# Performance work log

Hardware: AMD Instinct MI355X
Metric: run time of the kernel (lower is better)

The kernel has to match this reference:

```python
import jax, jax.numpy as jnp
import numpy as np

DT = 0.03125                                   # ray-march step size
NSTEPS = int(np.ceil(2.0 * np.sqrt(3.0) / DT)) # enough steps to cross the [-1,1]^3 cube diagonal (=111)


def trilinear_sample(vol, pos):
    """vol: [C, D, Hv, Wv]; pos: [H, W, 3] xyz in [-1,1] (grid_sample convention,
    align_corners=True). Returns [C, H, W]."""
    D, Hv, Wv = vol.shape[1], vol.shape[2], vol.shape[3]

    def axis(g, n):
        g = jnp.clip((g + 1.0) * 0.5 * (n - 1), 0.0, n - 1.0)
        i0 = jnp.minimum(jnp.floor(g).astype(jnp.int32), n - 2)
        return i0, i0 + 1, (g - i0)[None]  # frac broadcast over channel dim

    x0, x1, fx = axis(pos[..., 0], Wv)
    y0, y1, fy = axis(pos[..., 1], Hv)
    z0, z1, fz = axis(pos[..., 2], D)

    def g(z, y, x):
        return vol[:, z, y, x]  # [C, H, W]

    c00 = g(z0, y0, x0) * (1 - fx) + g(z0, y0, x1) * fx
    c01 = g(z0, y1, x0) * (1 - fx) + g(z0, y1, x1) * fx
    c10 = g(z1, y0, x0) * (1 - fx) + g(z1, y0, x1) * fx
    c11 = g(z1, y1, x0) * (1 - fx) + g(z1, y1, x1) * fx
    c0 = c00 * (1 - fy) + c01 * fy
    c1 = c10 * (1 - fy) + c11 * fy
    return c0 * (1 - fz) + c1 * fz


def setup_inputs() -> dict:
    key = jax.random.key(0)
    B, H, W, D = 2, 256, 256, 128
    camrot = jnp.tile(jnp.eye(3, dtype=jnp.float32)[None], (B, 1, 1))
    campos = jnp.tile(jnp.array([[0.0, 0.0, -2.5]], dtype=jnp.float32), (B, 1))
    focal = jnp.full((B, 2), 300.0, dtype=jnp.float32)
    princpt = jnp.full((B, 2), 128.0, dtype=jnp.float32)
    ys, xs = jnp.meshgrid(jnp.arange(H, dtype=jnp.float32),
                          jnp.arange(W, dtype=jnp.float32), indexing='ij')
    pixelcoords = jnp.tile(jnp.stack([xs, ys], axis=-1)[None], (B, 1, 1, 1))
    volume = jax.random.uniform(key, (B, 4, D, D, D), dtype=jnp.float32)
    return dict(camrot=camrot, campos=campos, focal=focal, princpt=princpt,
                pixelcoords=pixelcoords, volume=volume)


def reference(camrot, campos, focal, princpt, pixelcoords, volume):
    # camera rays: pixel -> camera -> world (camrot^T applied, as in torch sum over dim=-2)
    raydir = (pixelcoords - princpt[:, None, None, :]) / focal[:, None, None, :]
    raydir = jnp.concatenate([raydir, jnp.ones_like(raydir[..., :1])], axis=-1)
    raydir = jnp.einsum('bij,bhwi->bhwj', camrot, raydir)
    raydir = raydir / jnp.sqrt(jnp.sum(raydir ** 2, axis=-1, keepdims=True))

    # ray-AABB intersection with [-1,1]^3 (no grad, as in torch.no_grad())
    t1 = (-1.0 - campos[:, None, None, :]) / raydir
    t2 = (1.0 - campos[:, None, None, :]) / raydir
    tmin = jnp.maximum(jnp.minimum(t1[..., 0], t2[..., 0]),
                       jnp.maximum(jnp.minimum(t1[..., 1], t2[..., 1]),
                                   jnp.minimum(t1[..., 2], t2[..., 2])))
    tmax = jnp.minimum(jnp.maximum(t1[..., 0], t2[..., 0]),
                       jnp.minimum(jnp.maximum(t1[..., 1], t2[..., 1]),
                                   jnp.maximum(t1[..., 2], t2[..., 2])))
    hit = tmin < tmax
    t0 = jax.lax.stop_gradient(jnp.maximum(jnp.where(hit, tmin, 0.0), 0.0))

    raypos = campos[:, None, None, :] + raydir * t0[..., None]  # [B,H,W,3]
    B, H, W = raypos.shape[:3]
    rayrgb = jnp.zeros((B, 3, H, W), raypos.dtype)
    rayalpha = jnp.zeros((B, 1, H, W), raypos.dtype)

    def step(carry, _):
        raypos, rayrgb, rayalpha = carry
        valid = jnp.all((raypos > -1.0) & (raypos < 1.0), axis=-1).astype(raypos.dtype)
        samp = jax.vmap(trilinear_sample)(volume, raypos)  # [B,4,H,W]
        contrib = (jnp.minimum(rayalpha + samp[:, 3:4] * DT, 1.0) - rayalpha) * valid[:, None]
        rayrgb = rayrgb + samp[:, :3] * contrib
        rayalpha = rayalpha + contrib
        raypos = raypos + raydir * DT
        return (raypos, rayrgb, rayalpha), None

    (_, rayrgb, rayalpha), _ = jax.lax.scan(step, (raypos, rayrgb, rayalpha),
                                            None, length=NSTEPS)
    return jnp.concatenate([rayrgb, rayalpha], axis=1)  # [B,4,H,W]
```

## Files before the change

### kernel.cpp

```cpp
#include <hip/hip_runtime.h>
#include <math.h>

#pragma clang fp contract(off)

#define DT 0.03125f
#define NSTEPS 111

__device__ __forceinline__ float4 lerp4(float4 a, float4 b, float w) {
#pragma clang fp contract(off)
    float wa = 1.0f - w;
    float4 r;
    r.x = a.x * wa + b.x * w;
    r.y = a.y * wa + b.y * w;
    r.z = a.z * wa + b.z * w;
    r.w = a.w * wa + b.w * w;
    return r;
}


__global__ __launch_bounds__(256) void repack4_kernel(const float* __restrict__ vol,
                                                      float4* __restrict__ out,
                                                      long spatial) {
    long q = (long)blockIdx.x * blockDim.x + threadIdx.x;
    long nq = spatial >> 2;
    if (q >= nq) return;
    long b = blockIdx.y;
    const float* p = vol + b * 4 * spatial + (q << 2);
    float4 c0 = *(const float4*)(p);
    float4 c1 = *(const float4*)(p + spatial);
    float4 c2 = *(const float4*)(p + 2 * spatial);
    float4 c3 = *(const float4*)(p + 3 * spatial);
    float4* o = out + b * spatial + (q << 2);
    o[0] = make_float4(c0.x, c1.x, c2.x, c3.x);
    o[1] = make_float4(c0.y, c1.y, c2.y, c3.y);
    o[2] = make_float4(c0.z, c1.z, c2.z, c3.z);
    o[3] = make_float4(c0.w, c1.w, c2.w, c3.w);
}

__global__ __launch_bounds__(256) void repack_kernel(const float* __restrict__ vol,
                                                     float4* __restrict__ out,
                                                     long total, long spatial) {
    long idx = (long)blockIdx.x * blockDim.x + threadIdx.x;
    if (idx >= total) return;
    long b = idx / spatial;
    long s = idx - b * spatial;
    const float* p = vol + b * 4 * spatial + s;
    float4 v;
    v.x = p[0];
    v.y = p[spatial];
    v.z = p[2 * spatial];
    v.w = p[3 * spatial];
    out[idx] = v;
}


__device__ __forceinline__ int voxel_base(float posx, float posy, float posz,
                                          int D, float gmax, int zstride,
                                          float& fx, float& fy, float& fz) {
#pragma clang fp contract(off)
    float gx = fminf(fmaxf((posx + 1.0f) * 0.5f * gmax, 0.0f), gmax);
    float gy = fminf(fmaxf((posy + 1.0f) * 0.5f * gmax, 0.0f), gmax);
    float gz = fminf(fmaxf((posz + 1.0f) * 0.5f * gmax, 0.0f), gmax);
    int ix0 = (int)floorf(gx); if (ix0 > D - 2) ix0 = D - 2;
    int iy0 = (int)floorf(gy); if (iy0 > D - 2) iy0 = D - 2;
    int iz0 = (int)floorf(gz); if (iz0 > D - 2) iz0 = D - 2;
    fx = gx - (float)ix0;
    fy = gy - (float)iy0;
    fz = gz - (float)iz0;
    return iz0 * zstride + iy0 * D + ix0;
}

__device__ __forceinline__ void load8(const float4* __restrict__ v4, int base,
                                      int D, int zstride, float4* c) {
    c[0] = v4[base];
    c[1] = v4[base + 1];
    c[2] = v4[base + D];
    c[3] = v4[base + D + 1];
    c[4] = v4[base + zstride];
    c[5] = v4[base + zstride + 1];
    c[6] = v4[base + zstride + D];
    c[7] = v4[base + zstride + D + 1];
}

__device__ __forceinline__ void accum_step(const float4* c, float fx, float fy, float fz,
                                           float& accr, float& accg, float& accb,
                                           float& alpha) {
#pragma clang fp contract(off)
    float4 c00 = lerp4(c[0], c[1], fx);
    float4 c01 = lerp4(c[2], c[3], fx);
    float4 c10 = lerp4(c[4], c[5], fx);
    float4 c11 = lerp4(c[6], c[7], fx);
    float4 c0 = lerp4(c00, c01, fy);
    float4 c1 = lerp4(c10, c11, fy);
    float4 samp = lerp4(c0, c1, fz);
    float contrib = fminf(alpha + samp.w * DT, 1.0f) - alpha;
    accr = accr + samp.x * contrib;
    accg = accg + samp.y * contrib;
    accb = accb + samp.z * contrib;
    alpha = alpha + contrib;
}

__global__ __launch_bounds__(256, 1) void raymarch_pipe_kernel(
        const float* __restrict__ camrot, const float* __restrict__ campos,
        const float* __restrict__ focal, const float* __restrict__ princpt,
        const float* __restrict__ pixelcoords, const float4* __restrict__ vol4,
        float* __restrict__ out, int B, int H, int W, int D) {
#pragma clang fp contract(off)
    int x = blockIdx.x * blockDim.x + threadIdx.x;
    int y = blockIdx.y * blockDim.y + threadIdx.y;
    int b = blockIdx.z;
    if (x >= W || y >= H) return;

    long pidx = (((long)b * H + y) * W + x) * 2;
    float px = pixelcoords[pidx];
    float py = pixelcoords[pidx + 1];
    const float* R = camrot + b * 9;
    float cpx = campos[b * 3 + 0], cpy = campos[b * 3 + 1], cpz = campos[b * 3 + 2];
    float flx = focal[b * 2 + 0], fly = focal[b * 2 + 1];
    float prx = princpt[b * 2 + 0], pry = princpt[b * 2 + 1];

    float rx = (px - prx) / flx;
    float ry = (py - pry) / fly;
    float rz = 1.0f;
    float dx = R[0] * rx + R[3] * ry + R[6] * rz;
    float dy = R[1] * rx + R[4] * ry + R[7] * rz;
    float dz = R[2] * rx + R[5] * ry + R[8] * rz;
    float ss = dx * dx;
    ss = ss + dy * dy;
    ss = ss + dz * dz;
    float nrm = sqrtf(ss);
    dx = dx / nrm; dy = dy / nrm; dz = dz / nrm;

    float t1x = (-1.0f - cpx) / dx, t2x = (1.0f - cpx) / dx;
    float t1y = (-1.0f - cpy) / dy, t2y = (1.0f - cpy) / dy;
    float t1z = (-1.0f - cpz) / dz, t2z = (1.0f - cpz) / dz;
    float tmin = fmaxf(fminf(t1x, t2x), fmaxf(fminf(t1y, t2y), fminf(t1z, t2z)));
    float tmax = fminf(fmaxf(t1x, t2x), fminf(fmaxf(t1y, t2y), fmaxf(t1z, t2z)));
    bool hit = tmin < tmax;
    float t0 = fmaxf(hit ? tmin : 0.0f, 0.0f);

    float posx = cpx + dx * t0;
    float posy = cpy + dy * t0;
    float posz = cpz + dz * t0;
    float stx = dx * DT, sty = dy * DT, stz = dz * DT;

    int n = 0;
    float e0x = 0.0f, e0y = 0.0f, e0z = 0.0f;
    {
        float sx = posx, sy = posy, sz = posz;
        int firstv = -1;
        for (int s = 0; s < NSTEPS; ++s) {
            bool valid = (sx > -1.0f) && (sx < 1.0f) &&
                         (sy > -1.0f) && (sy < 1.0f) &&
                         (sz > -1.0f) && (sz < 1.0f);
            if (valid) {
                if (firstv < 0) { firstv = s; e0x = sx; e0y = sy; e0z = sz; }
                n++;
            } else if (firstv >= 0) {
                break;
            }
            sx = sx + stx; sy = sy + sty; sz = sz + stz;
        }
    }

    float accr = 0.0f, accg = 0.0f, accb = 0.0f, alpha = 0.0f;
    float gmax = (float)(D - 1);
    int zstride = D * D;
    int spatial = zstride * D;
    const float4* v4b = vol4 + (long)b * spatial;

    if (n > 0) {
        float pxx = e0x, pyy = e0y, pzz = e0z;
        float fxA, fyA, fzA, fxB = 0.f, fyB = 0.f, fzB = 0.f;
        float4 A[8], Bv[8];

        int baseA = voxel_base(pxx, pyy, pzz, D, gmax, zstride, fxA, fyA, fzA);
        load8(v4b, baseA, D, zstride, A);
        pxx = pxx + stx; pyy = pyy + sty; pzz = pzz + stz;

        if (n > 1) {
            int baseB = voxel_base(pxx, pyy, pzz, D, gmax, zstride, fxB, fyB, fzB);
            load8(v4b, baseB, D, zstride, Bv);
            pxx = pxx + stx; pyy = pyy + sty; pzz = pzz + stz;
        }

        int i = 0;
        for (; i + 2 < n; i += 2) {
            accum_step(A, fxA, fyA, fzA, accr, accg, accb, alpha);
            int baseA2 = voxel_base(pxx, pyy, pzz, D, gmax, zstride, fxA, fyA, fzA);
            load8(v4b, baseA2, D, zstride, A);
            pxx = pxx + stx; pyy = pyy + sty; pzz = pzz + stz;

            accum_step(Bv, fxB, fyB, fzB, accr, accg, accb, alpha);
            int baseB2 = voxel_base(pxx, pyy, pzz, D, gmax, zstride, fxB, fyB, fzB);
            load8(v4b, baseB2, D, zstride, Bv);
            pxx = pxx + stx; pyy = pyy + sty; pzz = pzz + stz;
        }
        if (i < n) { accum_step(A, fxA, fyA, fzA, accr, accg, accb, alpha); i++; }
        if (i < n) { accum_step(Bv, fxB, fyB, fzB, accr, accg, accb, alpha); }
    }

    long hw = (long)H * W;
    long o = (long)b * 4 * hw + (long)y * W + x;
    out[o] = accr;
    out[o + hw] = accg;
    out[o + 2 * hw] = accb;
    out[o + 3 * hw] = alpha;
}

__global__ __launch_bounds__(256) void raymarch_simple_kernel(
        const float* __restrict__ camrot, const float* __restrict__ campos,
        const float* __restrict__ focal, const float* __restrict__ princpt,
        const float* __restrict__ pixelcoords, const float* __restrict__ vol,
        float* __restrict__ out, int B, int H, int W, int D) {
#pragma clang fp contract(off)
    int x = blockIdx.x * blockDim.x + threadIdx.x;
    int y = blockIdx.y * blockDim.y + threadIdx.y;
    int b = blockIdx.z;
    if (x >= W || y >= H) return;

    long pidx = (((long)b * H + y) * W + x) * 2;
    float px = pixelcoords[pidx];
    float py = pixelcoords[pidx + 1];
    const float* R = camrot + b * 9;
    float cpx = campos[b * 3 + 0], cpy = campos[b * 3 + 1], cpz = campos[b * 3 + 2];
    float flx = focal[b * 2 + 0], fly = focal[b * 2 + 1];
    float prx = princpt[b * 2 + 0], pry = princpt[b * 2 + 1];

    float rx = (px - prx) / flx;
    float ry = (py - pry) / fly;
    float rz = 1.0f;
    float dx = R[0] * rx + R[3] * ry + R[6] * rz;
    float dy = R[1] * rx + R[4] * ry + R[7] * rz;
    float dz = R[2] * rx + R[5] * ry + R[8] * rz;
    float ss = dx * dx;
    ss = ss + dy * dy;
    ss = ss + dz * dz;
    float nrm = sqrtf(ss);
    dx = dx / nrm; dy = dy / nrm; dz = dz / nrm;

    float t1x = (-1.0f - cpx) / dx, t2x = (1.0f - cpx) / dx;
    float t1y = (-1.0f - cpy) / dy, t2y = (1.0f - cpy) / dy;
    float t1z = (-1.0f - cpz) / dz, t2z = (1.0f - cpz) / dz;
    float tmin = fmaxf(fminf(t1x, t2x), fmaxf(fminf(t1y, t2y), fminf(t1z, t2z)));
    float tmax = fminf(fmaxf(t1x, t2x), fminf(fmaxf(t1y, t2y), fmaxf(t1z, t2z)));
    bool hit = tmin < tmax;
    float t0 = fmaxf(hit ? tmin : 0.0f, 0.0f);

    float posx = cpx + dx * t0;
    float posy = cpy + dy * t0;
    float posz = cpz + dz * t0;
    float stx = dx * DT, sty = dy * DT, stz = dz * DT;

    float accr = 0.0f, accg = 0.0f, accb = 0.0f, alpha = 0.0f;
    float gmax = (float)(D - 1);
    long spatial = (long)D * D * D;
    long zstride = (long)D * D;
    const float* vb = vol + (long)b * 4 * spatial;

    bool entered = false;
    for (int s = 0; s < NSTEPS; ++s) {
        bool valid = (posx > -1.0f) && (posx < 1.0f) &&
                     (posy > -1.0f) && (posy < 1.0f) &&
                     (posz > -1.0f) && (posz < 1.0f);
        if (valid) {
            entered = true;
            float gx = fminf(fmaxf((posx + 1.0f) * 0.5f * gmax, 0.0f), gmax);
            float gy = fminf(fmaxf((posy + 1.0f) * 0.5f * gmax, 0.0f), gmax);
            float gz = fminf(fmaxf((posz + 1.0f) * 0.5f * gmax, 0.0f), gmax);
            int ix0 = (int)floorf(gx); if (ix0 > D - 2) ix0 = D - 2;
            int iy0 = (int)floorf(gy); if (iy0 > D - 2) iy0 = D - 2;
            int iz0 = (int)floorf(gz); if (iz0 > D - 2) iz0 = D - 2;
            float fx = gx - (float)ix0;
            float fy = gy - (float)iy0;
            float fz = gz - (float)iz0;

            long s000 = (long)iz0 * zstride + (long)iy0 * D + ix0;
            float4 c000, c001, c010, c011, c100, c101, c110, c111;
            #define FETCH(dst, off) { long o_ = (off); \
                dst.x = vb[o_]; dst.y = vb[o_ + spatial]; \
                dst.z = vb[o_ + 2 * spatial]; dst.w = vb[o_ + 3 * spatial]; }
            FETCH(c000, s000);
            FETCH(c001, s000 + 1);
            FETCH(c010, s000 + D);
            FETCH(c011, s000 + D + 1);
            FETCH(c100, s000 + zstride);
            FETCH(c101, s000 + zstride + 1);
            FETCH(c110, s000 + zstride + D);
            FETCH(c111, s000 + zstride + D + 1);
            #undef FETCH
            float4 c00 = lerp4(c000, c001, fx);
            float4 c01 = lerp4(c010, c011, fx);
            float4 c10 = lerp4(c100, c101, fx);
            float4 c11 = lerp4(c110, c111, fx);
            float4 c0 = lerp4(c00, c01, fy);
            float4 c1 = lerp4(c10, c11, fy);
            float4 samp = lerp4(c0, c1, fz);

            float contrib = fminf(alpha + samp.w * DT, 1.0f) - alpha;
            accr = accr + samp.x * contrib;
            accg = accg + samp.y * contrib;
            accb = accb + samp.z * contrib;
            alpha = alpha + contrib;
            if (alpha >= 1.0f) break;
        } else if (entered) {
            break;
        }
        posx = posx + stx; posy = posy + sty; posz = posz + stz;
    }

    long hw = (long)H * W;
    long o = (long)b * 4 * hw + (long)y * W + x;
    out[o] = accr;
    out[o + hw] = accg;
    out[o + 2 * hw] = accb;
    out[o + 3 * hw] = alpha;
}

extern "C" void kernel_launch(void* const* d_in, const int* in_sizes, int n_in,
                              void* d_out, int out_size, void* d_ws, size_t ws_size,
                              hipStream_t stream) {
    const float* camrot = (const float*)d_in[0];
    const float* campos = (const float*)d_in[1];
    const float* focal = (const float*)d_in[2];
    const float* princpt = (const float*)d_in[3];
    const float* pixelcoords = (const float*)d_in[4];
    const float* volume = (const float*)d_in[5];
    float* out = (float*)d_out;

    int B = in_sizes[0] / 9;
    long spatial = (long)in_sizes[5] / (B * 4);
    int D = (int)lround(cbrt((double)spatial));
    while ((long)D * D * D > spatial) D--;
    while ((long)(D + 1) * (D + 1) * (D + 1) <= spatial) D++;
    long hw = (long)in_sizes[4] / (B * 2);
    int H = (int)lround(sqrt((double)hw));
    int W = H;

    size_t need = (size_t)B * spatial * 4 * sizeof(float);
    dim3 blk(16, 16, 1);
    dim3 grd((W + 15) / 16, (H + 15) / 16, B);

    if (ws_size >= need) {
        if ((spatial & 3) == 0) {
            long nq = spatial >> 2;
            dim3 rgrd((unsigned)((nq + 255) / 256), B, 1);
            repack4_kernel<<<rgrd, dim3(256), 0, stream>>>(volume, (float4*)d_ws, spatial);
        } else {
            long total = (long)B * spatial;
            repack_kernel<<<dim3((unsigned)((total + 255) / 256)), dim3(256), 0, stream>>>(
                volume, (float4*)d_ws, total, spatial);
        }
        raymarch_pipe_kernel<<<grd, blk, 0, stream>>>(camrot, campos, focal, princpt,
                                                      pixelcoords, (const float4*)d_ws,
                                                      out, B, H, W, D);
    } else {
        raymarch_simple_kernel<<<grd, blk, 0, stream>>>(camrot, campos, focal, princpt,
                                                        pixelcoords, volume,
                                                        out, B, H, W, D);
    }
}
```

Before: 165.1 us.

## Deepen ray-march prefetch to four stages, compute step count analytically, shrink blocks

Replaces the serial pre-scan that counted valid steps with an analytic step count derived from the slab intersection (tmax - t0) plus a margin. Validity becomes a per-step 0/1 mask that multiplies the contribution. Load pipelining goes from two in-flight sample sets to four, and the kernel is templated on D=128 so index arithmetic folds to constants. Blocks shrink to 16x4 threads with launch_bounds(64,2). Together these aim to remove the pre-scan loop and hide more gather latency, at the cost of more registers (32 float4s in flight) and some wasted masked loads past the ray's exit.

```diff
diff --git a/kernel.cpp b/kernel.cpp
--- a/kernel.cpp
+++ b/kernel.cpp
@@ -4,6 +4,7 @@
 #pragma clang fp contract(off)
 
 #define DT 0.03125f
+#define INV_DT 32.0f
 #define NSTEPS 111
 
 __device__ __forceinline__ float4 lerp4(float4 a, float4 b, float w) {
@@ -54,37 +55,9 @@
 }
 
 
-__device__ __forceinline__ int voxel_base(float posx, float posy, float posz,
-                                          int D, float gmax, int zstride,
-                                          float& fx, float& fy, float& fz) {
-#pragma clang fp contract(off)
-    float gx = fminf(fmaxf((posx + 1.0f) * 0.5f * gmax, 0.0f), gmax);
-    float gy = fminf(fmaxf((posy + 1.0f) * 0.5f * gmax, 0.0f), gmax);
-    float gz = fminf(fmaxf((posz + 1.0f) * 0.5f * gmax, 0.0f), gmax);
-    int ix0 = (int)floorf(gx); if (ix0 > D - 2) ix0 = D - 2;
-    int iy0 = (int)floorf(gy); if (iy0 > D - 2) iy0 = D - 2;
-    int iz0 = (int)floorf(gz); if (iz0 > D - 2) iz0 = D - 2;
-    fx = gx - (float)ix0;
-    fy = gy - (float)iy0;
-    fz = gz - (float)iz0;
-    return iz0 * zstride + iy0 * D + ix0;
-}
-
-__device__ __forceinline__ void load8(const float4* __restrict__ v4, int base,
-                                      int D, int zstride, float4* c) {
-    c[0] = v4[base];
-    c[1] = v4[base + 1];
-    c[2] = v4[base + D];
-    c[3] = v4[base + D + 1];
-    c[4] = v4[base + zstride];
-    c[5] = v4[base + zstride + 1];
-    c[6] = v4[base + zstride + D];
-    c[7] = v4[base + zstride + D + 1];
-}
-
 __device__ __forceinline__ void accum_step(const float4* c, float fx, float fy, float fz,
-                                           float& accr, float& accg, float& accb,
-                                           float& alpha) {
+                                           float m, float& accr, float& accg,
+                                           float& accb, float& alpha) {
 #pragma clang fp contract(off)
     float4 c00 = lerp4(c[0], c[1], fx);
     float4 c01 = lerp4(c[2], c[3], fx);
@@ -93,21 +66,23 @@
     float4 c0 = lerp4(c00, c01, fy);
     float4 c1 = lerp4(c10, c11, fy);
     float4 samp = lerp4(c0, c1, fz);
-    float contrib = fminf(alpha + samp.w * DT, 1.0f) - alpha;
+    float contrib = (fminf(alpha + samp.w * DT, 1.0f) - alpha) * m;
     accr = accr + samp.x * contrib;
     accg = accg + samp.y * contrib;
     accb = accb + samp.z * contrib;
     alpha = alpha + contrib;
 }
 
-__global__ __launch_bounds__(256, 1) void raymarch_pipe_kernel(
+template <int DD>
+__global__ __launch_bounds__(64, 2) void raymarch_pipe_kernel(
         const float* __restrict__ camrot, const float* __restrict__ campos,
         const float* __restrict__ focal, const float* __restrict__ princpt,
         const float* __restrict__ pixelcoords, const float4* __restrict__ vol4,
-        float* __restrict__ out, int B, int H, int W, int D) {
-#pragma clang fp contract(off)
-    int x = blockIdx.x * blockDim.x + threadIdx.x;
-    int y = blockIdx.y * blockDim.y + threadIdx.y;
+        float* __restrict__ out, int B, int H, int W, int Drt) {
+#pragma clang fp contract(off)
+    const int D = (DD > 0) ? DD : Drt;
+    int x = blockIdx.x * 16 + threadIdx.x;
+    int y = blockIdx.y * 4 + threadIdx.y;
     int b = blockIdx.z;
     if (x >= W || y >= H) return;
 
@@ -144,60 +119,59 @@
     float posz = cpz + dz * t0;
     float stx = dx * DT, sty = dy * DT, stz = dz * DT;
 
-    int n = 0;
-    float e0x = 0.0f, e0y = 0.0f, e0z = 0.0f;
-    {
-        float sx = posx, sy = posy, sz = posz;
-        int firstv = -1;
-        for (int s = 0; s < NSTEPS; ++s) {
-            bool valid = (sx > -1.0f) && (sx < 1.0f) &&
-                         (sy > -1.0f) && (sy < 1.0f) &&
-                         (sz > -1.0f) && (sz < 1.0f);
-            if (valid) {
-                if (firstv < 0) { firstv = s; e0x = sx; e0y = sy; e0z = sz; }
-                n++;
-            } else if (firstv >= 0) {
-                break;
-            }
-            sx = sx + stx; sy = sy + sty; sz = sz + stz;
-        }
-    }
+    float span = (tmax - t0) * INV_DT + 4.0f;
+    span = fminf(span, (float)NSTEPS);
+    int n = (hit && span > 0.0f) ? (int)span : 0;
 
     float accr = 0.0f, accg = 0.0f, accb = 0.0f, alpha = 0.0f;
     float gmax = (float)(D - 1);
-    int zstride = D * D;
-    int spatial = zstride * D;
-    const float4* v4b = vol4 + (long)b * spatial;
+    const int zstride = D * D;
+    const float4* v4b = vol4 + (long)b * ((long)zstride * D);
 
     if (n > 0) {
-        float pxx = e0x, pyy = e0y, pzz = e0z;
-        float fxA, fyA, fzA, fxB = 0.f, fyB = 0.f, fzB = 0.f;
-        float4 A[8], Bv[8];
-
-        int baseA = voxel_base(pxx, pyy, pzz, D, gmax, zstride, fxA, fyA, fzA);
-        load8(v4b, baseA, D, zstride, A);
-        pxx = pxx + stx; pyy = pyy + sty; pzz = pzz + stz;
-
-        if (n > 1) {
-            int baseB = voxel_base(pxx, pyy, pzz, D, gmax, zstride, fxB, fyB, fzB);
-            load8(v4b, baseB, D, zstride, Bv);
-            pxx = pxx + stx; pyy = pyy + sty; pzz = pzz + stz;
+        float pxx = posx, pyy = posy, pzz = posz;
+        int spf = 0;
+        float4 C0[8], C1[8], C2[8], C3[8];
+        float f0x, f0y, f0z, m0, f1x, f1y, f1z, m1;
+        float f2x, f2y, f2z, m2, f3x, f3y, f3z, m3;
+
+#define PREFETCH(CC, FX, FY, FZ, M) do {                                        \
+        bool inside = (pxx > -1.0f) && (pxx < 1.0f) && (pyy > -1.0f) &&         \
+                      (pyy < 1.0f) && (pzz > -1.0f) && (pzz < 1.0f);            \
+        M = (inside && (spf < NSTEPS)) ? 1.0f : 0.0f;                           \
+        float gx = fminf(fmaxf((pxx + 1.0f) * 0.5f * gmax, 0.0f), gmax);        \
+        float gy = fminf(fmaxf((pyy + 1.0f) * 0.5f * gmax, 0.0f), gmax);        \
+        float gz = fminf(fmaxf((pzz + 1.0f) * 0.5f * gmax, 0.0f), gmax);        \
+        int ix0 = (int)floorf(gx); if (ix0 > D - 2) ix0 = D - 2;                \
+        int iy0 = (int)floorf(gy); if (iy0 > D - 2) iy0 = D - 2;                \
+        int iz0 = (int)floorf(gz); if (iz0 > D - 2) iz0 = D - 2;                \
+        FX = gx - (float)ix0; FY = gy - (float)iy0; FZ = gz - (float)iz0;       \
+        int base = iz0 * zstride + iy0 * D + ix0;                               \
+        CC[0] = v4b[base];                CC[1] = v4b[base + 1];                \
+        CC[2] = v4b[base + D];            CC[3] = v4b[base + D + 1];            \
+        CC[4] = v4b[base + zstride];      CC[5] = v4b[base + zstride + 1];      \
+        CC[6] = v4b[base + zstride + D];  CC[7] = v4b[base + zstride + D + 1];  \
+        pxx = pxx + stx; pyy = pyy + sty; pzz = pzz + stz;                      \
+        spf = spf + 1;                                                          \
+    } while (0)
+
+        PREFETCH(C0, f0x, f0y, f0z, m0);
+        PREFETCH(C1, f1x, f1y, f1z, m1);
+        PREFETCH(C2, f2x, f2y, f2z, m2);
+        PREFETCH(C3, f3x, f3y, f3z, m3);
+
+        int iters = (n + 3) >> 2;
+        for (int it = 0; it < iters; ++it) {
+            accum_step(C0, f0x, f0y, f0z, m0, accr, accg, accb, alpha);
+            PREFETCH(C0, f0x, f0y, f0z, m0);
+            accum_step(C1, f1x, f1y, f1z, m1, accr, accg, accb, alpha);
+            PREFETCH(C1, f1x, f1y, f1z, m1);
+            accum_step(C2, f2x, f2y, f2z, m2, accr, accg, accb, alpha);
+            PREFETCH(C2, f2x, f2y, f2z, m2);
+            accum_step(C3, f3x, f3y, f3z, m3, accr, accg, accb, alpha);
+            PREFETCH(C3, f3x, f3y, f3z, m3);
         }
-
-        int i = 0;
-        for (; i + 2 < n; i += 2) {
-            accum_step(A, fxA, fyA, fzA, accr, accg, accb, alpha);
-            int baseA2 = voxel_base(pxx, pyy, pzz, D, gmax, zstride, fxA, fyA, fzA);
-            load8(v4b, baseA2, D, zstride, A);
-            pxx = pxx + stx; pyy = pyy + sty; pzz = pzz + stz;
-
-            accum_step(Bv, fxB, fyB, fzB, accr, accg, accb, alpha);
-            int baseB2 = voxel_base(pxx, pyy, pzz, D, gmax, zstride, fxB, fyB, fzB);
-            load8(v4b, baseB2, D, zstride, Bv);
-            pxx = pxx + stx; pyy = pyy + sty; pzz = pzz + stz;
-        }
-        if (i < n) { accum_step(A, fxA, fyA, fzA, accr, accg, accb, alpha); i++; }
-        if (i < n) { accum_step(Bv, fxB, fyB, fzB, accr, accg, accb, alpha); }
+#undef PREFETCH
     }
 
     long hw = (long)H * W;
@@ -338,8 +312,6 @@
     int W = H;
 
     size_t need = (size_t)B * spatial * 4 * sizeof(float);
-    dim3 blk(16, 16, 1);
-    dim3 grd((W + 15) / 16, (H + 15) / 16, B);
 
     if (ws_size >= need) {
         if ((spatial & 3) == 0) {
@@ -351,10 +323,20 @@
             repack_kernel<<<dim3((unsigned)((total + 255) / 256)), dim3(256), 0, stream>>>(
                 volume, (float4*)d_ws, total, spatial);
         }
-        raymarch_pipe_kernel<<<grd, blk, 0, stream>>>(camrot, campos, focal, princpt,
-                                                      pixelcoords, (const float4*)d_ws,
-                                                      out, B, H, W, D);
+        dim3 blk(16, 4, 1);
+        dim3 grd((W + 15) / 16, (H + 3) / 4, B);
+        if (D == 128) {
+            raymarch_pipe_kernel<128><<<grd, blk, 0, stream>>>(
+                camrot, campos, focal, princpt, pixelcoords, (const float4*)d_ws,
+                out, B, H, W, D);
+        } else {
+            raymarch_pipe_kernel<0><<<grd, blk, 0, stream>>>(
+                camrot, campos, focal, princpt, pixelcoords, (const float4*)d_ws,
+                out, B, H, W, D);
+        }
     } else {
+        dim3 blk(16, 16, 1);
+        dim3 grd((W + 15) / 16, (H + 15) / 16, B);
         raymarch_simple_kernel<<<grd, blk, 0, stream>>>(camrot, campos, focal, princpt,
                                                         pixelcoords, volume,
                                                         out, B, H, W, D);
```

Result: no change. 162.9 us (-1.3%).
